# Kernel optimization log

Hardware: AMD Instinct MI355X
Metric: run time of the kernel (lower is better)

The kernel has to match this reference:

```python
import jax, jax.numpy as jnp
import numpy as np

VOCAB, DIM, HEADS, LAYERS = 32000, 1024, 16, 2
B, S = 2, 1024
HD = DIM // HEADS


def rmsnorm(x, g, eps=1e-6):
    return x * jax.lax.rsqrt(jnp.mean(x * x, axis=-1, keepdims=True) + eps) * g


def setup_inputs() -> dict:
    key = jax.random.key(0)
    ks = jax.random.split(key, 20)
    s = 0.02
    d = {
        "text_ids": jax.random.randint(ks[0], (B, S), 0, VOCAB),
        "embed": jax.random.normal(ks[1], (VOCAB, DIM), jnp.float32) * s,
        "g1": jnp.ones((LAYERS, DIM), jnp.float32),
        "wq": jax.random.normal(ks[2], (LAYERS, DIM, DIM), jnp.float32) * s,
        "bq": jnp.zeros((LAYERS, DIM), jnp.float32),
        "wk": jax.random.normal(ks[3], (LAYERS, DIM, DIM), jnp.float32) * s,
        "bk": jnp.zeros((LAYERS, DIM), jnp.float32),
        "wv": jax.random.normal(ks[4], (LAYERS, DIM, DIM), jnp.float32) * s,
        "bv": jnp.zeros((LAYERS, DIM), jnp.float32),
        "wo": jax.random.normal(ks[5], (LAYERS, DIM, DIM), jnp.float32) * s,
        "bo": jnp.zeros((LAYERS, DIM), jnp.float32),
        "g2": jnp.ones((LAYERS, DIM), jnp.float32),
        "w1": jax.random.normal(ks[6], (LAYERS, DIM, 4 * DIM), jnp.float32) * s,
        "b1": jnp.zeros((LAYERS, 4 * DIM), jnp.float32),
        "w2": jax.random.normal(ks[7], (LAYERS, 4 * DIM, DIM), jnp.float32) * s,
        "b2": jnp.zeros((LAYERS, DIM), jnp.float32),
        "gf": jnp.ones((DIM,), jnp.float32),
        "head_w": jax.random.normal(ks[8], (DIM, VOCAB), jnp.float32) * s,
        "head_b": jnp.zeros((VOCAB,), jnp.float32),
    }
    return d


def reference(text_ids, embed, g1, wq, bq, wk, bk, wv, bv, wo, bo,
              g2, w1, b1, w2, b2, gf, head_w, head_b):
    b, s = text_ids.shape
    x = embed[text_ids]                                   # [B,S,D]
    causal = jnp.tril(jnp.ones((s, s), dtype=bool))        # [S,S]
    scale = 1.0 / jnp.sqrt(jnp.asarray(HD, x.dtype))
    for l in range(LAYERS):
        # attention sublayer: x = x + attn(norm1(x))
        h = rmsnorm(x, g1[l])
        q = (h @ wq[l] + bq[l]).reshape(b, s, HEADS, HD)
        k = (h @ wk[l] + bk[l]).reshape(b, s, HEADS, HD)
        v = (h @ wv[l] + bv[l]).reshape(b, s, HEADS, HD)
        scores = jnp.einsum("bqhd,bkhd->bhqk", q, k) * scale
        scores = jnp.where(causal, scores, jnp.asarray(-1e30, scores.dtype))
        a = jax.nn.softmax(scores, axis=-1)
        o = jnp.einsum("bhqk,bkhd->bqhd", a, v).reshape(b, s, DIM)
        x = x + (o @ wo[l] + bo[l])
        # FFN sublayer: x = x + ffn(norm2(x)), SiLU MLP (MoE unused in source forward)
        h2 = rmsnorm(x, g2[l])
        x = x + (jax.nn.silu(h2 @ w1[l] + b1[l]) @ w2[l] + b2[l])
    x = rmsnorm(x, gf)
    return x.astype(jnp.float32) @ head_w + head_b         # [B,S,VOCAB]
```

## Files before the change

### kernel.cpp

```cpp
#include <hip/hip_runtime.h>

#define LAYERS 2
#define DIM 1024
#define HEADS 16
#define HD 64
#define BATCH 2
#define SEQ 1024
#define ROWS (BATCH * SEQ)
#define FFN (4 * DIM)
#define VOCAB 32000
#define QKVN (3 * DIM)

typedef unsigned short u16;
typedef short vshort8 __attribute__((ext_vector_type(8)));
typedef float f32x4 __attribute__((ext_vector_type(4)));

#define VMCNT(n) asm volatile("s_waitcnt vmcnt(" #n ")" ::: "memory")

__device__ __forceinline__ u16 f2bf(float f) {
  union { float f; unsigned u; } x{f};
  unsigned r = (x.u + 0x7fffu + ((x.u >> 16) & 1u)) >> 16;
  return (u16)r;
}

// ... 8 lines not shown
  int xcd = orig & 7;
  int base = (xcd < r) ? xcd * (q + 1) : r * (q + 1) + (xcd - r) * q;
  return base + (orig >> 3);
}

__device__ __forceinline__ void trans64(const float* __restrict__ src,
                                        u16* __restrict__ dst, int C, int R,
                                        int r0, int c0, int tid,
                                        u16 (*tl)[72]) {
  int lr = tid >> 4, lc4 = (tid & 15) * 4;
#pragma unroll
  for (int i = 0; i < 4; i++) {
    int row = lr + i * 16;
    float4 v = *(const float4*)&src[(size_t)(r0 + row) * C + c0 + lc4];
    ushort4 o{f2bf(v.x), f2bf(v.y), f2bf(v.z), f2bf(v.w)};
    *(ushort4*)&tl[row][lc4] = o;
  }
  __syncthreads();
#pragma unroll
  for (int i = 0; i < 2; i++) {
    int idx = tid + i * 256;
    int ci = idx >> 3, ri0 = (idx & 7) * 8;
    vshort8 o;
#pragma unroll
    for (int j = 0; j < 8; j++) o[j] = (short)tl[ri0 + j][ci];
    *(vshort8*)&dst[(size_t)(c0 + ci) * R + r0 + ri0] = o;
  }
}

__global__ __launch_bounds__(256) void transpose_all_kernel(
    const float* __restrict__ wq, const float* __restrict__ wk,
    const float* __restrict__ wv, const float* __restrict__ wo,
    const float* __restrict__ w1, const float* __restrict__ w2,
    const float* __restrict__ head_w, u16* __restrict__ wqkvT,
    u16* __restrict__ woT, u16* __restrict__ w1T, u16* __restrict__ w2T,
    u16* __restrict__ headT) {
  __shared__ u16 tl[64][72];
  int bid = blockIdx.x, tid = threadIdx.x;
  const float* src;
  u16* dst;
  int R, C, r0, c0;
  if (bid < 2048) {
    int job = bid >> 8, tile = bid & 255;
    int l = job >> 2, wsel = job & 3;
    src = (wsel == 0 ? wq : wsel == 1 ? wk : wsel == 2 ? wv : wo) +
          (size_t)l * DIM * DIM;
    dst = (wsel < 3)
              ? wqkvT + (size_t)l * QKVN * DIM + (size_t)wsel * DIM * DIM
              : woT + (size_t)l * DIM * DIM;
    R = DIM; C = DIM;
    c0 = (tile & 15) * 64; r0 = (tile >> 4) * 64;
  } else if (bid < 4096) {
    int idx = bid - 2048;
    int l = idx >> 10, t = idx & 1023;
    src = w1 + (size_t)l * DIM * FFN;
    dst = w1T + (size_t)l * DIM * FFN;
    R = DIM; C = FFN;
    c0 = (t & 63) * 64; r0 = (t >> 6) * 64;
  } else if (bid < 6144) {
    int idx = bid - 4096;
    int l = idx >> 10, t = idx & 1023;
    src = w2 + (size_t)l * FFN * DIM;
    dst = w2T + (size_t)l * FFN * DIM;
    R = FFN; C = DIM;
    c0 = (t & 15) * 64; r0 = (t >> 4) * 64;
  } else {
    int t = bid - 6144;
    src = head_w; dst = headT;
    R = DIM; C = VOCAB;
    c0 = (t % 500) * 64; r0 = (t / 500) * 64;
  }
  trans64(src, dst, C, R, r0, c0, tid, tl);
}

__global__ __launch_bounds__(256) void pack_qkv_bias(
    const float* __restrict__ bq, const float* __restrict__ bk,
    const float* __restrict__ bv, float* __restrict__ o) {
  int l = blockIdx.y;
  int t = blockIdx.x * 256 + threadIdx.x;
  float v;
  if (t < DIM) v = bq[l * DIM + t];
  else if (t < 2 * DIM) v = bk[l * DIM + t - DIM];
  else v = bv[l * DIM + t - 2 * DIM];
  o[(size_t)l * QKVN + t] = v;
}

__global__ __launch_bounds__(256) void embed_norm_kernel(
    const int* __restrict__ ids, const float* __restrict__ emb,
    const float* __restrict__ g, float* __restrict__ x, u16* __restrict__ h) {
  int row = blockIdx.x;
  int t = threadIdx.x;
  int id = ids[row];
  float4 v = ((const float4*)(emb + (size_t)id * DIM))[t];
  ((float4*)(x + (size_t)row * DIM))[t] = v;
  float ss = v.x * v.x + v.y * v.y + v.z * v.z + v.w * v.w;
  for (int off = 32; off > 0; off >>= 1) ss += __shfl_down(ss, off);
  __shared__ float part[4];
  if ((t & 63) == 0) part[t >> 6] = ss;
  __syncthreads();
  float tot = part[0] + part[1] + part[2] + part[3];
  float r = rsqrtf(tot / (float)DIM + 1e-6f);
  float4 gv = ((const float4*)g)[t];
  ushort4 o;
  o.x = f2bf(v.x * r * gv.x);
  o.y = f2bf(v.y * r * gv.y);
  o.z = f2bf(v.z * r * gv.z);
  o.w = f2bf(v.w * r * gv.w);
  *(ushort4*)(h + (size_t)row * DIM + t * 4) = o;
}

__global__ __launch_bounds__(256) void addnorm_kernel(
    float* __restrict__ x, const float* __restrict__ P0,
    const float* __restrict__ P1, const float* __restrict__ bias,
    const float* __restrict__ g, u16* __restrict__ h) {
  int row = blockIdx.x;
  int t = threadIdx.x;
  float4 v = ((const float4*)(x + (size_t)row * DIM))[t];
  float4 a = ((const float4*)(P0 + (size_t)row * DIM))[t];
  float4 b = ((const float4*)(P1 + (size_t)row * DIM))[t];
  float4 c = ((const float4*)bias)[t];
  v.x += a.x + b.x + c.x;
  v.y += a.y + b.y + c.y;
  v.z += a.z + b.z + c.z;
  v.w += a.w + b.w + c.w;
  ((float4*)(x + (size_t)row * DIM))[t] = v;
  float ss = v.x * v.x + v.y * v.y + v.z * v.z + v.w * v.w;
  for (int off = 32; off > 0; off >>= 1) ss += __shfl_down(ss, off);
  __shared__ float part[4];
  if ((t & 63) == 0) part[t >> 6] = ss;
  __syncthreads();
  float tot = part[0] + part[1] + part[2] + part[3];
  float r = rsqrtf(tot / (float)DIM + 1e-6f);
  float4 gv = ((const float4*)g)[t];
  ushort4 o;
  o.x = f2bf(v.x * r * gv.x);
  o.y = f2bf(v.y * r * gv.y);
  o.z = f2bf(v.z * r * gv.z);
  o.w = f2bf(v.w * r * gv.w);
  *(ushort4*)(h + (size_t)row * DIM + t * 4) = o;
}

template <int SILU, int VT>
__global__ __launch_bounds__(512, 2) void gemm256x128_kernel(
    const u16* __restrict__ A, const u16* __restrict__ Wt,
    const float* __restrict__ bias, u16* __restrict__ outb,
    u16* __restrict__ vt2, int M, int N, int K) {
  __shared__ u16 As[2][256 * 64];
  __shared__ u16 Bs[2][128 * 64];
  int nm = M >> 8, nn = N >> 7;
  int wg = xcd_swizzle(blockIdx.x, nm * nn);
  int mi = wg % nm, ni = wg / nm;
  int m0 = mi << 8, n0 = ni << 7;
  int tid = threadIdx.x, w = tid >> 6, lane = tid & 63;
  int wr = w >> 1, wc = w & 1;
  int r16 = lane & 15, g4 = lane >> 4;
  int srow8 = lane >> 3, sslot = lane & 7;
  int NT = K >> 6;

  f32x4 acc[4][4] = {};

  auto stageA = [&](int buf, int kt, int j) {
    int chunk = j * 8 + w;
    int row = chunk * 8 + srow8;
    int slot = sslot ^ (row & 7);
    gll16(A + (size_t)(m0 + row) * K + kt * 64 + slot * 8,
          &As[buf][chunk * 512 + lane * 8]);
  };
  auto stageB = [&](int buf, int kt, int j) {
    int chunk = j * 8 + w;
    int row = chunk * 8 + srow8;
    int slot = sslot ^ (row & 7);
    gll16(Wt + (size_t)(n0 + row) * K + kt * 64 + slot * 8,
          &Bs[buf][chunk * 512 + lane * 8]);
  };
  auto readA = [&](int buf, int mf, int kk) -> vshort8 {
    int row = wr * 64 + mf * 16 + r16;
    int slot = (kk * 4 + g4) ^ (row & 7);
    return *(const vshort8*)&As[buf][row * 64 + slot * 8];
  };
  auto readB = [&](int buf, int nf, int kk) -> vshort8 {
    int row = wc * 64 + nf * 16 + r16;
    int slot = (kk * 4 + g4) ^ (row & 7);
    return *(const vshort8*)&Bs[buf][row * 64 + slot * 8];
  };

  stageA(0, 0, 0); stageA(0, 0, 1); stageA(0, 0, 2); stageA(0, 0, 3);
  stageB(0, 0, 0); stageB(0, 0, 1);
  VMCNT(0);
  __builtin_amdgcn_s_barrier();

  vshort8 af[4][2], bf[2][2];

  for (int t = 0; t < NT; t++) {
    int cur = t & 1, nxt = cur ^ 1;
    bool hn = (t + 1 < NT);
#pragma unroll
    for (int m = 0; m < 4; m++)
#pragma unroll
      for (int kk = 0; kk < 2; kk++) af[m][kk] = readA(cur, m, kk);
#pragma unroll
    for (int n = 0; n < 2; n++)
#pragma unroll
      for (int kk = 0; kk < 2; kk++) bf[n][kk] = readB(cur, n, kk);
    if (hn) {
      stageA(nxt, t + 1, 0); stageA(nxt, t + 1, 1);
      stageA(nxt, t + 1, 2); stageA(nxt, t + 1, 3);
      stageB(nxt, t + 1, 0); stageB(nxt, t + 1, 1);
    }
    __builtin_amdgcn_s_barrier();
    __builtin_amdgcn_s_setprio(1);
#pragma unroll
    for (int m = 0; m < 4; m++)
#pragma unroll
      for (int n = 0; n < 2; n++)
#pragma unroll
        for (int kk = 0; kk < 2; kk++)
          acc[m][n] = __builtin_amdgcn_mfma_f32_16x16x32_bf16(
              af[m][kk], bf[n][kk], acc[m][n], 0, 0, 0);
    __builtin_amdgcn_s_setprio(0);
    __builtin_amdgcn_s_barrier();
#pragma unroll
    for (int n = 0; n < 2; n++)
#pragma unroll
      for (int kk = 0; kk < 2; kk++) bf[n][kk] = readB(cur, 2 + n, kk);
    __builtin_amdgcn_s_barrier();
    __builtin_amdgcn_s_setprio(1);
#pragma unroll
    for (int m = 0; m < 4; m++)
#pragma unroll
      for (int n = 0; n < 2; n++)
#pragma unroll
        for (int kk = 0; kk < 2; kk++)
          acc[m][n + 2] = __builtin_amdgcn_mfma_f32_16x16x32_bf16(
              af[m][kk], bf[n][kk], acc[m][n + 2], 0, 0, 0);
    __builtin_amdgcn_s_setprio(0);
    VMCNT(0);
    __builtin_amdgcn_s_barrier();
  }

#pragma unroll
  for (int m = 0; m < 4; m++) {
    int rowb = m0 + wr * 64 + m * 16 + g4 * 4;
#pragma unroll
    for (int n = 0; n < 4; n++) {
      int col = n0 + wc * 64 + n * 16 + r16;
      float b = bias[col];
      u16 ov[4];
#pragma unroll
      for (int j = 0; j < 4; j++) {
        float v = acc[m][n][j] + b;
        if (SILU) v = v / (1.f + __expf(-v));
        ov[j] = f2bf(v);
      }
      if (VT && col >= 2 * DIM) {
        int dv = col - 2 * DIM;
        int hh = dv >> 6, dd = dv & 63;
        int bb = rowb >> 10, s = rowb & 1023;
        ushort4 o4{ov[0], ov[1], ov[2], ov[3]};
        *(ushort4*)&vt2[((((size_t)(bb * 16 + hh) * (SEQ / 8) + (s >> 3)) * 64 +
                          dd) * 8) + (s & 7)] = o4;
      } else {
#pragma unroll
        for (int j = 0; j < 4; j++)
          outb[(size_t)(rowb + j) * N + col] = ov[j];
      }
    }
  }
}

template <int OUTBF, int SILU, int SPLITK, int MFAST, int VT>
__global__ __launch_bounds__(256, 2) void gemm128_kernel(
    const u16* __restrict__ A, const u16* __restrict__ Wt,
    const float* __restrict__ bias, void* __restrict__ outv,
    float* __restrict__ pout1, u16* __restrict__ vt2, int M, int N, int K) {
  __shared__ u16 As[2][128 * 64];
  __shared__ u16 Bs[2][128 * 64];
  int nm = M >> 7, nn = N >> 7, nwg = nm * nn;
  int wg = xcd_swizzle(blockIdx.x, SPLITK ? nwg * 2 : nwg);
  int ks = 0;
  if (SPLITK) { ks = wg >= nwg; wg -= ks * nwg; }
  int mi, ni;
  if (MFAST) { mi = wg % nm; ni = wg / nm; }
  else       { ni = wg % nn; mi = wg / nn; }
  int m0 = mi << 7, n0 = ni << 7;
  int kb = SPLITK ? ks * (K >> 1) : 0;
  int NTt = (SPLITK ? (K >> 1) : K) >> 6;
  int tid = threadIdx.x, wave = tid >> 6, lane = tid & 63;
  int wr = wave >> 1, wc = wave & 1;
  int r16 = lane & 15, g4 = lane >> 4;
  int lrow = lane >> 3, lslot = lane & 7;

  f32x4 acc[4][4] = {};

  auto stage = [&](int buf, int kt) {
#pragma unroll
    for (int i = 0; i < 4; i++) {
      int s = wave * 4 + i;
      int row = s * 8 + lrow;
      int slot = lslot ^ (row & 7);
      gll16(A + (size_t)(m0 + row) * K + kb + kt * 64 + slot * 8,
            &As[buf][s * 512 + lane * 8]);
    }
#pragma unroll
    for (int i = 0; i < 4; i++) {
      int s = wave * 4 + i;
      int row = s * 8 + lrow;
      int slot = lslot ^ (row & 7);
// ... 26 lines not shown
      }
#pragma unroll
      for (int m = 0; m < 4; m++)
#pragma unroll
        for (int n = 0; n < 4; n++)
          acc[m][n] = __builtin_amdgcn_mfma_f32_16x16x32_bf16(af[m], bf[n],
                                                              acc[m][n], 0, 0, 0);
    }
    VMCNT(0);
    __builtin_amdgcn_s_barrier();
  }

  if (SPLITK) {
    float* P = ks ? pout1 : (float*)outv;
#pragma unroll
    for (int m = 0; m < 4; m++) {
      int rowb = m0 + wr * 64 + m * 16 + g4 * 4;
#pragma unroll
      for (int n = 0; n < 4; n++) {
        int col = n0 + wc * 64 + n * 16 + r16;
#pragma unroll
        for (int j = 0; j < 4; j++)
          P[(size_t)(rowb + j) * N + col] = acc[m][n][j];
      }
    }
  } else {
#pragma unroll
    for (int m = 0; m < 4; m++) {
      int rowb = m0 + wr * 64 + m * 16 + g4 * 4;
#pragma unroll
      for (int n = 0; n < 4; n++) {
        int col = n0 + wc * 64 + n * 16 + r16;
        float b = bias[col];
        u16 ov[4];
#pragma unroll
        for (int j = 0; j < 4; j++) {
          float v = acc[m][n][j] + b;
          if (SILU) v = v / (1.f + __expf(-v));
          if (OUTBF) ov[j] = f2bf(v);
          else ((float*)outv)[(size_t)(rowb + j) * N + col] = v;
        }
        if (OUTBF) {
          if (VT && col >= 2 * DIM) {
            int dv = col - 2 * DIM;
            int hh = dv >> 6, dd = dv & 63;
            int bb = rowb >> 10, s = rowb & 1023;
            ushort4 o4{ov[0], ov[1], ov[2], ov[3]};
            *(ushort4*)&vt2[((((size_t)(bb * 16 + hh) * (SEQ / 8) + (s >> 3)) * 64 +
                              dd) * 8) + (s & 7)] = o4;
          } else {
#pragma unroll
            for (int j = 0; j < 4; j++)
              ((u16*)outv)[(size_t)(rowb + j) * N + col] = ov[j];
          }
        }
      }
    }
  }
}

__global__ __launch_bounds__(512, 2) void gemm256p_kernel(
    const u16* __restrict__ A, const u16* __restrict__ Wt,
    const float* __restrict__ bias, float* __restrict__ out,
    int M, int N, int K) {
  __shared__ u16 As[2][256 * 64];
  __shared__ u16 Bs[2][256 * 64];
  int nn = N >> 8;
  int wg = xcd_swizzle(blockIdx.x, nn * 2);
  int ni = wg >> 1, mhalf = wg & 1;
  int n0 = ni << 8;
  int tid = threadIdx.x, w = tid >> 6, lane = tid & 63;
  int wr = w >> 2, wc = w & 3;
  int r16 = lane & 15, g4 = lane >> 4;
  int srow8 = lane >> 3, sslot = lane & 7;
  const int NTK = 16;
  const int NGT = 64;

  f32x4 acc[8][4] = {};

  auto stageA = [&](int buf, int mb, int kt, int hb, int j) {
    int chunk = j * 8 + w;
    int row = hb * 128 + chunk * 8 + srow8;
    int slot = sslot ^ (row & 7);
    gll16(A + (size_t)(mb + row) * K + kt * 64 + slot * 8,
          &As[buf][hb * 8192 + chunk * 512 + lane * 8]);
  };
  auto stageB = [&](int buf, int kt, int hb, int j) {
    int chunk = j * 8 + w;
    int row = hb * 128 + chunk * 8 + srow8;
    int slot = sslot ^ (row & 7);
    gll16(Wt + (size_t)(n0 + row) * K + kt * 64 + slot * 8,
          &Bs[buf][hb * 8192 + chunk * 512 + lane * 8]);
  };
  auto readA = [&](int buf, int mf, int kk) -> vshort8 {
    int row = mf * 32 + wr * 16 + r16;
    int slot = (kk * 4 + g4) ^ (row & 7);
    return *(const vshort8*)&As[buf][row * 64 + slot * 8];
  };
  auto readB = [&](int buf, int nf, int kk) -> vshort8 {
    int row = nf * 64 + wc * 16 + r16;
    int slot = (kk * 4 + g4) ^ (row & 7);
    return *(const vshort8*)&Bs[buf][row * 64 + slot * 8];
  };

  int mb0 = (mhalf * 4) << 8;
  stageA(0, mb0, 0, 0, 0); stageA(0, mb0, 0, 0, 1);
  stageB(0, 0, 0, 0);      stageB(0, 0, 0, 1);
  stageB(0, 0, 1, 0);      stageB(0, 0, 1, 1);
  stageA(0, mb0, 0, 1, 0); stageA(0, mb0, 0, 1, 1);
  VMCNT(4);
  __builtin_amdgcn_s_barrier();

  vshort8 af[4][2], bf0[2][2], bf1[2][2];

  for (int ti = 0; ti < 4; ti++) {
    int m0 = (mhalf * 4 + ti) << 8;
    for (int tt = 0; tt < NTK; tt++) {
      int gt = ti * NTK + tt;
      int cur = gt & 1, nxt = cur ^ 1;
      int gt1 = gt + 1;
      bool hn = gt1 < NGT;
      int kt1 = gt1 & (NTK - 1);
      int mb1 = (mhalf * 4 + (gt1 >> 4)) << 8;
#pragma unroll
      for (int m = 0; m < 4; m++)
#pragma unroll
        for (int kk = 0; kk < 2; kk++) af[m][kk] = readA(cur, m, kk);
#pragma unroll
      for (int n = 0; n < 2; n++)
#pragma unroll
        for (int kk = 0; kk < 2; kk++) bf0[n][kk] = readB(cur, n, kk);
      if (hn) {
        stageA(nxt, mb1, kt1, 0, 0); stageA(nxt, mb1, kt1, 0, 1);
        stageB(nxt, kt1, 0, 0);      stageB(nxt, kt1, 0, 1);
      }
      __builtin_amdgcn_s_barrier();
      __builtin_amdgcn_s_setprio(1);
#pragma unroll
      for (int m = 0; m < 4; m++)
#pragma unroll
        for (int n = 0; n < 2; n++)
#pragma unroll
          for (int kk = 0; kk < 2; kk++)
            acc[m][n] = __builtin_amdgcn_mfma_f32_16x16x32_bf16(
                af[m][kk], bf0[n][kk], acc[m][n], 0, 0, 0);
      __builtin_amdgcn_s_setprio(0);
      VMCNT(4);
      __builtin_amdgcn_s_barrier();
#pragma unroll
      for (int n = 0; n < 2; n++)
#pragma unroll
        for (int kk = 0; kk < 2; kk++) bf1[n][kk] = readB(cur, 2 + n, kk);
      __builtin_amdgcn_s_barrier();
      __builtin_amdgcn_s_setprio(1);
#pragma unroll
      for (int m = 0; m < 4; m++)
#pragma unroll
        for (int n = 0; n < 2; n++)
#pragma unroll
          for (int kk = 0; kk < 2; kk++)
            acc[m][n + 2] = __builtin_amdgcn_mfma_f32_16x16x32_bf16(
                af[m][kk], bf1[n][kk], acc[m][n + 2], 0, 0, 0);
      __builtin_amdgcn_s_setprio(0);
      __builtin_amdgcn_s_barrier();
#pragma unroll
      for (int m = 0; m < 4; m++)
#pragma unroll
        for (int kk = 0; kk < 2; kk++) af[m][kk] = readA(cur, 4 + m, kk);
      if (hn) {
        stageB(nxt, kt1, 1, 0);      stageB(nxt, kt1, 1, 1);
        stageA(nxt, mb1, kt1, 1, 0); stageA(nxt, mb1, kt1, 1, 1);
      }
      __builtin_amdgcn_s_barrier();
      __builtin_amdgcn_s_setprio(1);
#pragma unroll
      for (int m = 0; m < 4; m++)
#pragma unroll
        for (int n = 0; n < 2; n++)
#pragma unroll
          for (int kk = 0; kk < 2; kk++)
            acc[m + 4][n + 2] = __builtin_amdgcn_mfma_f32_16x16x32_bf16(
                af[m][kk], bf1[n][kk], acc[m + 4][n + 2], 0, 0, 0);
#pragma unroll
      for (int m = 0; m < 4; m++)
#pragma unroll
        for (int n = 0; n < 2; n++)
#pragma unroll
          for (int kk = 0; kk < 2; kk++)
            acc[m + 4][n] = __builtin_amdgcn_mfma_f32_16x16x32_bf16(
                af[m][kk], bf0[n][kk], acc[m + 4][n], 0, 0, 0);
      __builtin_amdgcn_s_setprio(0);
      VMCNT(4);
      __builtin_amdgcn_s_barrier();
    }
#pragma unroll
    for (int mf = 0; mf < 8; mf++) {
      int rowb = m0 + mf * 32 + wr * 16 + g4 * 4;
#pragma unroll
      for (int nf = 0; nf < 4; nf++) {
        int col = n0 + nf * 64 + wc * 16 + r16;
        float b = bias[col];
#pragma unroll
        for (int j = 0; j < 4; j++)
          out[(size_t)(rowb + j) * N + col] = acc[mf][nf][j] + b;
      }
    }
#pragma unroll
    for (int mf = 0; mf < 8; mf++)
#pragma unroll
      for (int nf = 0; nf < 4; nf++) acc[mf][nf] = f32x4{0.f, 0.f, 0.f, 0.f};
  }
}

__global__ __launch_bounds__(256) void attn_kernel(const u16* __restrict__ qkv,
                                                   const u16* __restrict__ vt2,
                                                   u16* __restrict__ o) {
  __shared__ u16 Ks[2][32 * 64];
  __shared__ u16 pl[4][16 * 40];
  int qblk = blockIdx.x, bh = blockIdx.y;
  int b = bh >> 4, h = bh & 15;
  int tid = threadIdx.x, w = tid >> 6, lane = tid & 63;
  int r16 = lane & 15, g4 = lane >> 4;
  int q0 = qblk * 64 + w * 16;

  const u16* qrow = qkv + ((size_t)(b * SEQ) + q0 + r16) * QKVN + h * HD;
  vshort8 aq0 = *(const vshort8*)(qrow + g4 * 8);
  vshort8 aq1 = *(const vshort8*)(qrow + 32 + g4 * 8);

  float mrun[4], lrun[4];
  f32x4 accO[4];
#pragma unroll
  for (int j = 0; j < 4; j++) { mrun[j] = -1e30f; lrun[j] = 0.f; }
#pragma unroll
  for (int d = 0; d < 4; d++) accO[d] = f32x4{0.f, 0.f, 0.f, 0.f};

  int nkvT = qblk * 2 + 2;
  auto stageK = [&](int buf, int kt) {
    int row = tid >> 3;
    int slot = (tid & 7) ^ (row & 7);
    gll16(qkv + ((size_t)(b * SEQ) + kt * 32 + row) * QKVN + DIM + h * HD + slot * 8,
          &Ks[buf][w * 512 + lane * 8]);
  };
  stageK(0, 0);
// ... 79 lines not shown
  const float* g2 = (const float*)d_in[11];
  const float* w1 = (const float*)d_in[12];
  const float* b1 = (const float*)d_in[13];
  const float* w2 = (const float*)d_in[14];
  const float* b2 = (const float*)d_in[15];
  const float* gf = (const float*)d_in[16];
  const float* head_w = (const float*)d_in[17];
  const float* head_b = (const float*)d_in[18];
  float* out = (float*)d_out;

  char* ws = (char*)d_ws;
  size_t off = 0;
  auto alloc = [&](size_t bytes) -> char* {
    char* p = ws + off;
    off += (bytes + 255) & ~(size_t)255;
    return p;
  };
  u16* wqkvT = (u16*)alloc((size_t)LAYERS * QKVN * DIM * 2);
  u16* woT = (u16*)alloc((size_t)LAYERS * DIM * DIM * 2);
  u16* w1T = (u16*)alloc((size_t)LAYERS * DIM * FFN * 2);
  u16* w2T = (u16*)alloc((size_t)LAYERS * DIM * FFN * 2);
  u16* headT = (u16*)alloc((size_t)VOCAB * DIM * 2);
  float* bqkv = (float*)alloc((size_t)LAYERS * QKVN * 4);
  float* x = (float*)alloc((size_t)ROWS * DIM * 4);
  u16* h = (u16*)alloc((size_t)ROWS * DIM * 2);
  u16* qkvb = (u16*)alloc((size_t)ROWS * QKVN * 2);
  u16* vtb = (u16*)alloc((size_t)ROWS * DIM * 2);
  u16* ob = (u16*)alloc((size_t)ROWS * DIM * 2);
  u16* tb = (u16*)alloc((size_t)ROWS * FFN * 2);
  float* P0 = (float*)alloc((size_t)ROWS * DIM * 4);
  float* P1 = (float*)alloc((size_t)ROWS * DIM * 4);
  if (off > ws_size) return;

  transpose_all_kernel<<<14144, 256, 0, stream>>>(
      wq, wk, wv, wo, w1, w2, head_w, wqkvT, woT, w1T, w2T, headT);
  pack_qkv_bias<<<dim3(QKVN / 256, LAYERS), 256, 0, stream>>>(bq, bk, bv, bqkv);
  embed_norm_kernel<<<ROWS, 256, 0, stream>>>(ids, emb, g1, x, h);

  for (int l = 0; l < LAYERS; l++) {
    gemm256x128_kernel<0, 1>
        <<<(ROWS / 256) * (QKVN / 128), 512, 0, stream>>>(
            h, wqkvT + (size_t)l * QKVN * DIM, bqkv + (size_t)l * QKVN,
            qkvb, vtb, ROWS, QKVN, DIM);
    attn_kernel<<<dim3(SEQ / 64, BATCH * HEADS), 256, 0, stream>>>(qkvb, vtb, ob);
    gemm128_kernel<0, 0, 1, 0, 0>
        <<<2 * (ROWS / 128) * (DIM / 128), 256, 0, stream>>>(
            ob, woT + (size_t)l * DIM * DIM, nullptr, P0, P1, nullptr,
            ROWS, DIM, DIM);
    addnorm_kernel<<<ROWS, 256, 0, stream>>>(
        x, P0, P1, bo + (size_t)l * DIM, g2 + (size_t)l * DIM, h);
    gemm256x128_kernel<1, 0>
        <<<(ROWS / 256) * (FFN / 128), 512, 0, stream>>>(
            h, w1T + (size_t)l * DIM * FFN, b1 + (size_t)l * FFN, tb, nullptr,
            ROWS, FFN, DIM);
    gemm128_kernel<0, 0, 1, 0, 0>
        <<<2 * (ROWS / 128) * (DIM / 128), 256, 0, stream>>>(
            tb, w2T + (size_t)l * DIM * FFN, nullptr, P0, P1, nullptr,
            ROWS, DIM, FFN);
    addnorm_kernel<<<ROWS, 256, 0, stream>>>(
        x, P0, P1, b2 + (size_t)l * DIM,
        (l == LAYERS - 1) ? gf : (g1 + (size_t)(l + 1) * DIM), h);
  }
  gemm256p_kernel<<<(VOCAB / 256) * 2, 512, 0, stream>>>(
      h, headT, head_b, out, ROWS, VOCAB, DIM);
}
```

Baseline: 589.6 us.

## Triple-buffer 256x128 GEMM and reuse it persistently for the LM head

The 256x128 GEMM moves from double- to triple-buffered LDS, prefetching two K-tiles ahead with a partial vmcnt wait instead of a full drain every iteration. It also gains an NMT template parameter so one workgroup walks several M tiles for a fixed N column. The LM head now uses this kernel (NMT=8, 250 workgroups with 128-wide N tiles) in place of the dedicated 256x256 gemm256p kernel. Tripling LDS (144KB) may cut occupancy, and the head's smaller N tile lowers per-block reuse of the A operand.

```diff
diff --git a/kernel.cpp b/kernel.cpp
--- a/kernel.cpp
+++ b/kernel.cpp
@@ -172,38 +172,48 @@
   *(ushort4*)(h + (size_t)row * DIM + t * 4) = o;
 }
 
-template <int SILU, int VT>
-__global__ __launch_bounds__(512, 2) void gemm256x128_kernel(
+template <int NMT, int OUTF32, int SILU, int VT>
+__global__ __launch_bounds__(512, 2) void gemm256x128p_kernel(
     const u16* __restrict__ A, const u16* __restrict__ Wt,
-    const float* __restrict__ bias, u16* __restrict__ outb,
+    const float* __restrict__ bias, void* __restrict__ outv,
     u16* __restrict__ vt2, int M, int N, int K) {
-  __shared__ u16 As[2][256 * 64];
-  __shared__ u16 Bs[2][128 * 64];
+  __shared__ u16 As[3][256 * 64];
+  __shared__ u16 Bs[3][128 * 64];
   int nm = M >> 8, nn = N >> 7;
-  int wg = xcd_swizzle(blockIdx.x, nm * nn);
-  int mi = wg % nm, ni = wg / nm;
-  int m0 = mi << 8, n0 = ni << 7;
+  int nwg = (NMT == 1) ? nm * nn : nn;
+  int wg = xcd_swizzle(blockIdx.x, nwg);
+  int mi0, ni;
+  if (NMT == 1) { mi0 = wg % nm; ni = wg / nm; }
+  else          { mi0 = 0; ni = wg; }
+  int n0 = ni << 7;
   int tid = threadIdx.x, w = tid >> 6, lane = tid & 63;
   int wr = w >> 1, wc = w & 1;
   int r16 = lane & 15, g4 = lane >> 4;
   int srow8 = lane >> 3, sslot = lane & 7;
-  int NT = K >> 6;
+  const int NG = NMT * 16;
 
   f32x4 acc[4][4] = {};
 
-  auto stageA = [&](int buf, int kt, int j) {
-    int chunk = j * 8 + w;
-    int row = chunk * 8 + srow8;
-    int slot = sslot ^ (row & 7);
-    gll16(A + (size_t)(m0 + row) * K + kt * 64 + slot * 8,
-          &As[buf][chunk * 512 + lane * 8]);
-  };
-  auto stageB = [&](int buf, int kt, int j) {
-    int chunk = j * 8 + w;
-    int row = chunk * 8 + srow8;
-    int slot = sslot ^ (row & 7);
-    gll16(Wt + (size_t)(n0 + row) * K + kt * 64 + slot * 8,
-          &Bs[buf][chunk * 512 + lane * 8]);
+  auto stage = [&](int g) {
+    int buf = g % 3;
+    int kt = g & 15;
+    int mb = (mi0 + (g >> 4)) << 8;
+#pragma unroll
+    for (int j = 0; j < 4; j++) {
+      int chunk = j * 8 + w;
+      int row = chunk * 8 + srow8;
+      int slot = sslot ^ (row & 7);
+      gll16(A + (size_t)(mb + row) * K + kt * 64 + slot * 8,
+            &As[buf][chunk * 512 + lane * 8]);
+    }
+#pragma unroll
+    for (int j = 0; j < 2; j++) {
+      int chunk = j * 8 + w;
+      int row = chunk * 8 + srow8;
+      int slot = sslot ^ (row & 7);
+      gll16(Wt + (size_t)(n0 + row) * K + kt * 64 + slot * 8,
+            &Bs[buf][chunk * 512 + lane * 8]);
+    }
   };
   auto readA = [&](int buf, int mf, int kk) -> vshort8 {
     int row = wr * 64 + mf * 16 + r16;
@@ -216,85 +226,91 @@
     return *(const vshort8*)&Bs[buf][row * 64 + slot * 8];
   };
 
-  stageA(0, 0, 0); stageA(0, 0, 1); stageA(0, 0, 2); stageA(0, 0, 3);
-  stageB(0, 0, 0); stageB(0, 0, 1);
-  VMCNT(0);
+  stage(0);
+  stage(1);
+  VMCNT(6);
   __builtin_amdgcn_s_barrier();
 
-  vshort8 af[4][2], bf[2][2];
-
-  for (int t = 0; t < NT; t++) {
-    int cur = t & 1, nxt = cur ^ 1;
-    bool hn = (t + 1 < NT);
-#pragma unroll
-    for (int m = 0; m < 4; m++)
-#pragma unroll
-      for (int kk = 0; kk < 2; kk++) af[m][kk] = readA(cur, m, kk);
-#pragma unroll
-    for (int n = 0; n < 2; n++)
-#pragma unroll
-      for (int kk = 0; kk < 2; kk++) bf[n][kk] = readB(cur, n, kk);
-    if (hn) {
-      stageA(nxt, t + 1, 0); stageA(nxt, t + 1, 1);
-      stageA(nxt, t + 1, 2); stageA(nxt, t + 1, 3);
-      stageB(nxt, t + 1, 0); stageB(nxt, t + 1, 1);
-    }
-    __builtin_amdgcn_s_barrier();
-    __builtin_amdgcn_s_setprio(1);
-#pragma unroll
-    for (int m = 0; m < 4; m++)
+  vshort8 af[4][2], bf0[2][2], bf1[2][2];
+
+  for (int mt = 0; mt < NMT; mt++) {
+    for (int kt = 0; kt < 16; kt++) {
+      int g = mt * 16 + kt;
+      int buf = g % 3;
+#pragma unroll
+      for (int m = 0; m < 4; m++)
+#pragma unroll
+        for (int kk = 0; kk < 2; kk++) af[m][kk] = readA(buf, m, kk);
 #pragma unroll
       for (int n = 0; n < 2; n++)
 #pragma unroll
-        for (int kk = 0; kk < 2; kk++)
-          acc[m][n] = __builtin_amdgcn_mfma_f32_16x16x32_bf16(
-              af[m][kk], bf[n][kk], acc[m][n], 0, 0, 0);
-    __builtin_amdgcn_s_setprio(0);
-    __builtin_amdgcn_s_barrier();
-#pragma unroll
-    for (int n = 0; n < 2; n++)
-#pragma unroll
-      for (int kk = 0; kk < 2; kk++) bf[n][kk] = readB(cur, 2 + n, kk);
-    __builtin_amdgcn_s_barrier();
-    __builtin_amdgcn_s_setprio(1);
-#pragma unroll
-    for (int m = 0; m < 4; m++)
+        for (int kk = 0; kk < 2; kk++) bf0[n][kk] = readB(buf, n, kk);
+      bool staged = (g + 2 < NG);
+      if (staged) stage(g + 2);
+      __builtin_amdgcn_s_barrier();
+      __builtin_amdgcn_s_setprio(1);
+#pragma unroll
+      for (int m = 0; m < 4; m++)
+#pragma unroll
+        for (int n = 0; n < 2; n++)
+#pragma unroll
+          for (int kk = 0; kk < 2; kk++)
+            acc[m][n] = __builtin_amdgcn_mfma_f32_16x16x32_bf16(
+                af[m][kk], bf0[n][kk], acc[m][n], 0, 0, 0);
+      __builtin_amdgcn_s_setprio(0);
+      __builtin_amdgcn_s_barrier();
 #pragma unroll
       for (int n = 0; n < 2; n++)
 #pragma unroll
-        for (int kk = 0; kk < 2; kk++)
-          acc[m][n + 2] = __builtin_amdgcn_mfma_f32_16x16x32_bf16(
-              af[m][kk], bf[n][kk], acc[m][n + 2], 0, 0, 0);
-    __builtin_amdgcn_s_setprio(0);
-    VMCNT(0);
-    __builtin_amdgcn_s_barrier();
-  }
-
-#pragma unroll
-  for (int m = 0; m < 4; m++) {
-    int rowb = m0 + wr * 64 + m * 16 + g4 * 4;
-#pragma unroll
-    for (int n = 0; n < 4; n++) {
-      int col = n0 + wc * 64 + n * 16 + r16;
-      float b = bias[col];
-      u16 ov[4];
-#pragma unroll
-      for (int j = 0; j < 4; j++) {
-        float v = acc[m][n][j] + b;
-        if (SILU) v = v / (1.f + __expf(-v));
-        ov[j] = f2bf(v);
-      }
-      if (VT && col >= 2 * DIM) {
-        int dv = col - 2 * DIM;
-        int hh = dv >> 6, dd = dv & 63;
-        int bb = rowb >> 10, s = rowb & 1023;
-        ushort4 o4{ov[0], ov[1], ov[2], ov[3]};
-        *(ushort4*)&vt2[((((size_t)(bb * 16 + hh) * (SEQ / 8) + (s >> 3)) * 64 +
-                          dd) * 8) + (s & 7)] = o4;
-      } else {
-#pragma unroll
-        for (int j = 0; j < 4; j++)
-          outb[(size_t)(rowb + j) * N + col] = ov[j];
+        for (int kk = 0; kk < 2; kk++) bf1[n][kk] = readB(buf, 2 + n, kk);
+      __builtin_amdgcn_s_barrier();
+      __builtin_amdgcn_s_setprio(1);
+#pragma unroll
+      for (int m = 0; m < 4; m++)
+#pragma unroll
+        for (int n = 0; n < 2; n++)
+#pragma unroll
+          for (int kk = 0; kk < 2; kk++)
+            acc[m][n + 2] = __builtin_amdgcn_mfma_f32_16x16x32_bf16(
+                af[m][kk], bf1[n][kk], acc[m][n + 2], 0, 0, 0);
+      __builtin_amdgcn_s_setprio(0);
+      if (staged) { VMCNT(6); } else { VMCNT(0); }
+      __builtin_amdgcn_s_barrier();
+    }
+    int m0e = (mi0 + mt) << 8;
+#pragma unroll
+    for (int m = 0; m < 4; m++) {
+      int rowb = m0e + wr * 64 + m * 16 + g4 * 4;
+#pragma unroll
+      for (int n = 0; n < 4; n++) {
+        int col = n0 + wc * 64 + n * 16 + r16;
+        float b = bias[col];
+        if (OUTF32) {
+#pragma unroll
+          for (int j = 0; j < 4; j++)
+            ((float*)outv)[(size_t)(rowb + j) * N + col] = acc[m][n][j] + b;
+        } else {
+          u16 ov[4];
+#pragma unroll
+          for (int j = 0; j < 4; j++) {
+            float v = acc[m][n][j] + b;
+            if (SILU) v = v / (1.f + __expf(-v));
+            ov[j] = f2bf(v);
+          }
+          if (VT && col >= 2 * DIM) {
+            int dv = col - 2 * DIM;
+            int hh = dv >> 6, dd = dv & 63;
+            int bb = rowb >> 10, s = rowb & 1023;
+            ushort4 o4{ov[0], ov[1], ov[2], ov[3]};
+            *(ushort4*)&vt2[((((size_t)(bb * 16 + hh) * (SEQ / 8) + (s >> 3)) *
+                                  64 + dd) * 8) + (s & 7)] = o4;
+          } else {
+#pragma unroll
+            for (int j = 0; j < 4; j++)
+              ((u16*)outv)[(size_t)(rowb + j) * N + col] = ov[j];
+          }
+        }
+        if (NMT > 1) acc[m][n] = f32x4{0.f, 0.f, 0.f, 0.f};
       }
     }
   }
@@ -406,174 +422,12 @@
           else ((float*)outv)[(size_t)(rowb + j) * N + col] = v;
         }
         if (OUTBF) {
-          if (VT && col >= 2 * DIM) {
-            int dv = col - 2 * DIM;
-            int hh = dv >> 6, dd = dv & 63;
-            int bb = rowb >> 10, s = rowb & 1023;
-            ushort4 o4{ov[0], ov[1], ov[2], ov[3]};
-            *(ushort4*)&vt2[((((size_t)(bb * 16 + hh) * (SEQ / 8) + (s >> 3)) * 64 +
-                              dd) * 8) + (s & 7)] = o4;
-          } else {
-#pragma unroll
-            for (int j = 0; j < 4; j++)
-              ((u16*)outv)[(size_t)(rowb + j) * N + col] = ov[j];
-          }
+#pragma unroll
+          for (int j = 0; j < 4; j++)
+            ((u16*)outv)[(size_t)(rowb + j) * N + col] = ov[j];
         }
       }
     }
-  }
-}
-
-__global__ __launch_bounds__(512, 2) void gemm256p_kernel(
-    const u16* __restrict__ A, const u16* __restrict__ Wt,
-    const float* __restrict__ bias, float* __restrict__ out,
-    int M, int N, int K) {
-  __shared__ u16 As[2][256 * 64];
-  __shared__ u16 Bs[2][256 * 64];
-  int nn = N >> 8;
-  int wg = xcd_swizzle(blockIdx.x, nn * 2);
-  int ni = wg >> 1, mhalf = wg & 1;
-  int n0 = ni << 8;
-  int tid = threadIdx.x, w = tid >> 6, lane = tid & 63;
-  int wr = w >> 2, wc = w & 3;
-  int r16 = lane & 15, g4 = lane >> 4;
-  int srow8 = lane >> 3, sslot = lane & 7;
-  const int NTK = 16;
-  const int NGT = 64;
-
-  f32x4 acc[8][4] = {};
-
-  auto stageA = [&](int buf, int mb, int kt, int hb, int j) {
-    int chunk = j * 8 + w;
-    int row = hb * 128 + chunk * 8 + srow8;
-    int slot = sslot ^ (row & 7);
-    gll16(A + (size_t)(mb + row) * K + kt * 64 + slot * 8,
-          &As[buf][hb * 8192 + chunk * 512 + lane * 8]);
-  };
-  auto stageB = [&](int buf, int kt, int hb, int j) {
-    int chunk = j * 8 + w;
-    int row = hb * 128 + chunk * 8 + srow8;
-    int slot = sslot ^ (row & 7);
-    gll16(Wt + (size_t)(n0 + row) * K + kt * 64 + slot * 8,
-          &Bs[buf][hb * 8192 + chunk * 512 + lane * 8]);
-  };
-  auto readA = [&](int buf, int mf, int kk) -> vshort8 {
-    int row = mf * 32 + wr * 16 + r16;
-    int slot = (kk * 4 + g4) ^ (row & 7);
-    return *(const vshort8*)&As[buf][row * 64 + slot * 8];
-  };
-  auto readB = [&](int buf, int nf, int kk) -> vshort8 {
-    int row = nf * 64 + wc * 16 + r16;
-    int slot = (kk * 4 + g4) ^ (row & 7);
-    return *(const vshort8*)&Bs[buf][row * 64 + slot * 8];
-  };
-
-  int mb0 = (mhalf * 4) << 8;
-  stageA(0, mb0, 0, 0, 0); stageA(0, mb0, 0, 0, 1);
-  stageB(0, 0, 0, 0);      stageB(0, 0, 0, 1);
-  stageB(0, 0, 1, 0);      stageB(0, 0, 1, 1);
-  stageA(0, mb0, 0, 1, 0); stageA(0, mb0, 0, 1, 1);
-  VMCNT(4);
-  __builtin_amdgcn_s_barrier();
-
-  vshort8 af[4][2], bf0[2][2], bf1[2][2];
-
-  for (int ti = 0; ti < 4; ti++) {
-    int m0 = (mhalf * 4 + ti) << 8;
-    for (int tt = 0; tt < NTK; tt++) {
-      int gt = ti * NTK + tt;
-      int cur = gt & 1, nxt = cur ^ 1;
-      int gt1 = gt + 1;
-      bool hn = gt1 < NGT;
-      int kt1 = gt1 & (NTK - 1);
-      int mb1 = (mhalf * 4 + (gt1 >> 4)) << 8;
-#pragma unroll
-      for (int m = 0; m < 4; m++)
-#pragma unroll
-        for (int kk = 0; kk < 2; kk++) af[m][kk] = readA(cur, m, kk);
-#pragma unroll
-      for (int n = 0; n < 2; n++)
-#pragma unroll
-        for (int kk = 0; kk < 2; kk++) bf0[n][kk] = readB(cur, n, kk);
-      if (hn) {
-        stageA(nxt, mb1, kt1, 0, 0); stageA(nxt, mb1, kt1, 0, 1);
-        stageB(nxt, kt1, 0, 0);      stageB(nxt, kt1, 0, 1);
-      }
-      __builtin_amdgcn_s_barrier();
-      __builtin_amdgcn_s_setprio(1);
-#pragma unroll
-      for (int m = 0; m < 4; m++)
-#pragma unroll
-        for (int n = 0; n < 2; n++)
-#pragma unroll
-          for (int kk = 0; kk < 2; kk++)
-            acc[m][n] = __builtin_amdgcn_mfma_f32_16x16x32_bf16(
-                af[m][kk], bf0[n][kk], acc[m][n], 0, 0, 0);
-      __builtin_amdgcn_s_setprio(0);
-      VMCNT(4);
-      __builtin_amdgcn_s_barrier();
-#pragma unroll
-      for (int n = 0; n < 2; n++)
-#pragma unroll
-        for (int kk = 0; kk < 2; kk++) bf1[n][kk] = readB(cur, 2 + n, kk);
-      __builtin_amdgcn_s_barrier();
-      __builtin_amdgcn_s_setprio(1);
-#pragma unroll
-      for (int m = 0; m < 4; m++)
-#pragma unroll
-        for (int n = 0; n < 2; n++)
-#pragma unroll
-          for (int kk = 0; kk < 2; kk++)
-            acc[m][n + 2] = __builtin_amdgcn_mfma_f32_16x16x32_bf16(
-                af[m][kk], bf1[n][kk], acc[m][n + 2], 0, 0, 0);
-      __builtin_amdgcn_s_setprio(0);
-      __builtin_amdgcn_s_barrier();
-#pragma unroll
-      for (int m = 0; m < 4; m++)
-#pragma unroll
-        for (int kk = 0; kk < 2; kk++) af[m][kk] = readA(cur, 4 + m, kk);
-      if (hn) {
-        stageB(nxt, kt1, 1, 0);      stageB(nxt, kt1, 1, 1);
-        stageA(nxt, mb1, kt1, 1, 0); stageA(nxt, mb1, kt1, 1, 1);
-      }
-      __builtin_amdgcn_s_barrier();
-      __builtin_amdgcn_s_setprio(1);
-#pragma unroll
-      for (int m = 0; m < 4; m++)
-#pragma unroll
-        for (int n = 0; n < 2; n++)
-#pragma unroll
-          for (int kk = 0; kk < 2; kk++)
-            acc[m + 4][n + 2] = __builtin_amdgcn_mfma_f32_16x16x32_bf16(
-                af[m][kk], bf1[n][kk], acc[m + 4][n + 2], 0, 0, 0);
-#pragma unroll
-      for (int m = 0; m < 4; m++)
-#pragma unroll
-        for (int n = 0; n < 2; n++)
-#pragma unroll
-          for (int kk = 0; kk < 2; kk++)
-            acc[m + 4][n] = __builtin_amdgcn_mfma_f32_16x16x32_bf16(
-                af[m][kk], bf0[n][kk], acc[m + 4][n], 0, 0, 0);
-      __builtin_amdgcn_s_setprio(0);
-      VMCNT(4);
-      __builtin_amdgcn_s_barrier();
-    }
-#pragma unroll
-    for (int mf = 0; mf < 8; mf++) {
-      int rowb = m0 + mf * 32 + wr * 16 + g4 * 4;
-#pragma unroll
-      for (int nf = 0; nf < 4; nf++) {
-        int col = n0 + nf * 64 + wc * 16 + r16;
-        float b = bias[col];
-#pragma unroll
-        for (int j = 0; j < 4; j++)
-          out[(size_t)(rowb + j) * N + col] = acc[mf][nf][j] + b;
-      }
-    }
-#pragma unroll
-    for (int mf = 0; mf < 8; mf++)
-#pragma unroll
-      for (int nf = 0; nf < 4; nf++) acc[mf][nf] = f32x4{0.f, 0.f, 0.f, 0.f};
   }
 }
 
@@ -725,7 +579,7 @@
   embed_norm_kernel<<<ROWS, 256, 0, stream>>>(ids, emb, g1, x, h);
 
   for (int l = 0; l < LAYERS; l++) {
-    gemm256x128_kernel<0, 1>
+    gemm256x128p_kernel<1, 0, 0, 1>
         <<<(ROWS / 256) * (QKVN / 128), 512, 0, stream>>>(
             h, wqkvT + (size_t)l * QKVN * DIM, bqkv + (size_t)l * QKVN,
             qkvb, vtb, ROWS, QKVN, DIM);
@@ -736,7 +590,7 @@
             ROWS, DIM, DIM);
     addnorm_kernel<<<ROWS, 256, 0, stream>>>(
         x, P0, P1, bo + (size_t)l * DIM, g2 + (size_t)l * DIM, h);
-    gemm256x128_kernel<1, 0>
+    gemm256x128p_kernel<1, 0, 1, 0>
         <<<(ROWS / 256) * (FFN / 128), 512, 0, stream>>>(
             h, w1T + (size_t)l * DIM * FFN, b1 + (size_t)l * FFN, tb, nullptr,
             ROWS, FFN, DIM);
@@ -748,6 +602,6 @@
         x, P0, P1, b2 + (size_t)l * DIM,
         (l == LAYERS - 1) ? gf : (g1 + (size_t)(l + 1) * DIM), h);
   }
-  gemm256p_kernel<<<(VOCAB / 256) * 2, 512, 0, stream>>>(
-      h, headT, head_b, out, ROWS, VOCAB, DIM);
-}
+  gemm256x128p_kernel<8, 1, 0, 0><<<VOCAB / 128, 512, 0, stream>>>(
+      h, headT, head_b, out, nullptr, ROWS, VOCAB, DIM);
+}
```

Result: slower. 649.3 us (+10.1%).

## Triple-buffer the 256x128 GEMM pipeline and fold bias packing into transpose

Applied to the files above, without the earlier changes.

The 256x128 GEMM used for the QKV and FFN-up projections now keeps three LDS stages and prefetches two K-tiles ahead. It waits with a partial vmcnt instead of draining all loads every iteration, so global-to-LDS latency is hidden further behind the MFMA work. The QKV bias packing kernel is merged into the weight transpose launch as extra blocks, removing one kernel launch. The LM-head GEMM's workgroup-to-tile mapping changes so the two M halves are split by block range instead of interleaved, which alters cache locality across XCDs. The larger LDS footprint (144KB per block) limits residency to one block per CU, and an unused multi-M-tile template option is added.

```diff
diff --git a/kernel.cpp b/kernel.cpp
--- a/kernel.cpp
+++ b/kernel.cpp
@@ -64,11 +64,23 @@
     const float* __restrict__ wq, const float* __restrict__ wk,
     const float* __restrict__ wv, const float* __restrict__ wo,
     const float* __restrict__ w1, const float* __restrict__ w2,
-    const float* __restrict__ head_w, u16* __restrict__ wqkvT,
-    u16* __restrict__ woT, u16* __restrict__ w1T, u16* __restrict__ w2T,
-    u16* __restrict__ headT) {
+    const float* __restrict__ head_w, const float* __restrict__ bq,
+    const float* __restrict__ bk, const float* __restrict__ bv,
+    u16* __restrict__ wqkvT, u16* __restrict__ woT, u16* __restrict__ w1T,
+    u16* __restrict__ w2T, u16* __restrict__ headT,
+    float* __restrict__ bqkv) {
   __shared__ u16 tl[64][72];
   int bid = blockIdx.x, tid = threadIdx.x;
+  if (bid >= 14144) {
+    int t = (bid - 14144) * 256 + tid;
+    int l = t / QKVN, c = t % QKVN;
+    float v;
+    if (c < DIM) v = bq[l * DIM + c];
+    else if (c < 2 * DIM) v = bk[l * DIM + c - DIM];
+    else v = bv[l * DIM + c - 2 * DIM];
+    bqkv[(size_t)l * QKVN + c] = v;
+    return;
+  }
   const float* src;
   u16* dst;
   int R, C, r0, c0;
@@ -105,18 +117,6 @@
   trans64(src, dst, C, R, r0, c0, tid, tl);
 }
 
-__global__ __launch_bounds__(256) void pack_qkv_bias(
-    const float* __restrict__ bq, const float* __restrict__ bk,
-    const float* __restrict__ bv, float* __restrict__ o) {
-  int l = blockIdx.y;
-  int t = blockIdx.x * 256 + threadIdx.x;
-  float v;
-  if (t < DIM) v = bq[l * DIM + t];
-  else if (t < 2 * DIM) v = bk[l * DIM + t - DIM];
-  else v = bv[l * DIM + t - 2 * DIM];
-  o[(size_t)l * QKVN + t] = v;
-}
-
 __global__ __launch_bounds__(256) void embed_norm_kernel(
     const int* __restrict__ ids, const float* __restrict__ emb,
     const float* __restrict__ g, float* __restrict__ x, u16* __restrict__ h) {
@@ -172,38 +172,48 @@
   *(ushort4*)(h + (size_t)row * DIM + t * 4) = o;
 }
 
-template <int SILU, int VT>
-__global__ __launch_bounds__(512, 2) void gemm256x128_kernel(
+template <int NMT, int OUTF32, int SILU, int VT>
+__global__ __launch_bounds__(512, 2) void gemm256x128p_kernel(
     const u16* __restrict__ A, const u16* __restrict__ Wt,
-    const float* __restrict__ bias, u16* __restrict__ outb,
+    const float* __restrict__ bias, void* __restrict__ outv,
     u16* __restrict__ vt2, int M, int N, int K) {
-  __shared__ u16 As[2][256 * 64];
-  __shared__ u16 Bs[2][128 * 64];
+  __shared__ u16 As[3][256 * 64];
+  __shared__ u16 Bs[3][128 * 64];
   int nm = M >> 8, nn = N >> 7;
-  int wg = xcd_swizzle(blockIdx.x, nm * nn);
-  int mi = wg % nm, ni = wg / nm;
-  int m0 = mi << 8, n0 = ni << 7;
+  int nwg = (NMT == 1) ? nm * nn : nn;
+  int wg = xcd_swizzle(blockIdx.x, nwg);
+  int mi0, ni;
+  if (NMT == 1) { mi0 = wg % nm; ni = wg / nm; }
+  else          { mi0 = 0; ni = wg; }
+  int n0 = ni << 7;
   int tid = threadIdx.x, w = tid >> 6, lane = tid & 63;
   int wr = w >> 1, wc = w & 1;
   int r16 = lane & 15, g4 = lane >> 4;
   int srow8 = lane >> 3, sslot = lane & 7;
-  int NT = K >> 6;
+  const int NG = NMT * 16;
 
   f32x4 acc[4][4] = {};
 
-  auto stageA = [&](int buf, int kt, int j) {
-    int chunk = j * 8 + w;
-    int row = chunk * 8 + srow8;
-    int slot = sslot ^ (row & 7);
-    gll16(A + (size_t)(m0 + row) * K + kt * 64 + slot * 8,
-          &As[buf][chunk * 512 + lane * 8]);
-  };
-  auto stageB = [&](int buf, int kt, int j) {
-    int chunk = j * 8 + w;
-    int row = chunk * 8 + srow8;
-    int slot = sslot ^ (row & 7);
-    gll16(Wt + (size_t)(n0 + row) * K + kt * 64 + slot * 8,
-          &Bs[buf][chunk * 512 + lane * 8]);
+  auto stage = [&](int g) {
+    int buf = g % 3;
+    int kt = g & 15;
+    int mb = (mi0 + (g >> 4)) << 8;
+#pragma unroll
+    for (int j = 0; j < 4; j++) {
+      int chunk = j * 8 + w;
+      int row = chunk * 8 + srow8;
+      int slot = sslot ^ (row & 7);
+      gll16(A + (size_t)(mb + row) * K + kt * 64 + slot * 8,
+            &As[buf][chunk * 512 + lane * 8]);
+    }
+#pragma unroll
+    for (int j = 0; j < 2; j++) {
+      int chunk = j * 8 + w;
+      int row = chunk * 8 + srow8;
+      int slot = sslot ^ (row & 7);
+      gll16(Wt + (size_t)(n0 + row) * K + kt * 64 + slot * 8,
+            &Bs[buf][chunk * 512 + lane * 8]);
+    }
   };
   auto readA = [&](int buf, int mf, int kk) -> vshort8 {
     int row = wr * 64 + mf * 16 + r16;
@@ -216,95 +226,101 @@
     return *(const vshort8*)&Bs[buf][row * 64 + slot * 8];
   };
 
-  stageA(0, 0, 0); stageA(0, 0, 1); stageA(0, 0, 2); stageA(0, 0, 3);
-  stageB(0, 0, 0); stageB(0, 0, 1);
-  VMCNT(0);
+  stage(0);
+  stage(1);
+  VMCNT(6);
   __builtin_amdgcn_s_barrier();
 
-  vshort8 af[4][2], bf[2][2];
-
-  for (int t = 0; t < NT; t++) {
-    int cur = t & 1, nxt = cur ^ 1;
-    bool hn = (t + 1 < NT);
-#pragma unroll
-    for (int m = 0; m < 4; m++)
-#pragma unroll
-      for (int kk = 0; kk < 2; kk++) af[m][kk] = readA(cur, m, kk);
-#pragma unroll
-    for (int n = 0; n < 2; n++)
-#pragma unroll
-      for (int kk = 0; kk < 2; kk++) bf[n][kk] = readB(cur, n, kk);
-    if (hn) {
-      stageA(nxt, t + 1, 0); stageA(nxt, t + 1, 1);
-      stageA(nxt, t + 1, 2); stageA(nxt, t + 1, 3);
-      stageB(nxt, t + 1, 0); stageB(nxt, t + 1, 1);
-    }
-    __builtin_amdgcn_s_barrier();
-    __builtin_amdgcn_s_setprio(1);
-#pragma unroll
-    for (int m = 0; m < 4; m++)
+  vshort8 af[4][2], bf0[2][2], bf1[2][2];
+
+  for (int mt = 0; mt < NMT; mt++) {
+    for (int kt = 0; kt < 16; kt++) {
+      int g = mt * 16 + kt;
+      int buf = g % 3;
+#pragma unroll
+      for (int m = 0; m < 4; m++)
+#pragma unroll
+        for (int kk = 0; kk < 2; kk++) af[m][kk] = readA(buf, m, kk);
 #pragma unroll
       for (int n = 0; n < 2; n++)
 #pragma unroll
-        for (int kk = 0; kk < 2; kk++)
-          acc[m][n] = __builtin_amdgcn_mfma_f32_16x16x32_bf16(
-              af[m][kk], bf[n][kk], acc[m][n], 0, 0, 0);
-    __builtin_amdgcn_s_setprio(0);
-    __builtin_amdgcn_s_barrier();
-#pragma unroll
-    for (int n = 0; n < 2; n++)
-#pragma unroll
-      for (int kk = 0; kk < 2; kk++) bf[n][kk] = readB(cur, 2 + n, kk);
-    __builtin_amdgcn_s_barrier();
-    __builtin_amdgcn_s_setprio(1);
-#pragma unroll
-    for (int m = 0; m < 4; m++)
+        for (int kk = 0; kk < 2; kk++) bf0[n][kk] = readB(buf, n, kk);
+      bool staged = (g + 2 < NG);
+      if (staged) stage(g + 2);
+      __builtin_amdgcn_s_barrier();
+      __builtin_amdgcn_s_setprio(1);
+#pragma unroll
+      for (int m = 0; m < 4; m++)
+#pragma unroll
+        for (int n = 0; n < 2; n++)
+#pragma unroll
+          for (int kk = 0; kk < 2; kk++)
+            acc[m][n] = __builtin_amdgcn_mfma_f32_16x16x32_bf16(
+                af[m][kk], bf0[n][kk], acc[m][n], 0, 0, 0);
+      __builtin_amdgcn_s_setprio(0);
+      __builtin_amdgcn_s_barrier();
 #pragma unroll
       for (int n = 0; n < 2; n++)
 #pragma unroll
-        for (int kk = 0; kk < 2; kk++)
-          acc[m][n + 2] = __builtin_amdgcn_mfma_f32_16x16x32_bf16(
-              af[m][kk], bf[n][kk], acc[m][n + 2], 0, 0, 0);
-    __builtin_amdgcn_s_setprio(0);
-    VMCNT(0);
-    __builtin_amdgcn_s_barrier();
-  }
-
-#pragma unroll
-  for (int m = 0; m < 4; m++) {
-    int rowb = m0 + wr * 64 + m * 16 + g4 * 4;
-#pragma unroll
-    for (int n = 0; n < 4; n++) {
-      int col = n0 + wc * 64 + n * 16 + r16;
-      float b = bias[col];
-      u16 ov[4];
-#pragma unroll
-      for (int j = 0; j < 4; j++) {
-        float v = acc[m][n][j] + b;
-        if (SILU) v = v / (1.f + __expf(-v));
-        ov[j] = f2bf(v);
-      }
-      if (VT && col >= 2 * DIM) {
-        int dv = col - 2 * DIM;
-        int hh = dv >> 6, dd = dv & 63;
-        int bb = rowb >> 10, s = rowb & 1023;
-        ushort4 o4{ov[0], ov[1], ov[2], ov[3]};
-        *(ushort4*)&vt2[((((size_t)(bb * 16 + hh) * (SEQ / 8) + (s >> 3)) * 64 +
-                          dd) * 8) + (s & 7)] = o4;
-      } else {
-#pragma unroll
-        for (int j = 0; j < 4; j++)
-          outb[(size_t)(rowb + j) * N + col] = ov[j];
-      }
-    }
-  }
-}
-
-template <int OUTBF, int SILU, int SPLITK, int MFAST, int VT>
+        for (int kk = 0; kk < 2; kk++) bf1[n][kk] = readB(buf, 2 + n, kk);
+      __builtin_amdgcn_s_barrier();
+      __builtin_amdgcn_s_setprio(1);
+#pragma unroll
+      for (int m = 0; m < 4; m++)
+#pragma unroll
+        for (int n = 0; n < 2; n++)
+#pragma unroll
+          for (int kk = 0; kk < 2; kk++)
+            acc[m][n + 2] = __builtin_amdgcn_mfma_f32_16x16x32_bf16(
+                af[m][kk], bf1[n][kk], acc[m][n + 2], 0, 0, 0);
+      __builtin_amdgcn_s_setprio(0);
+      if (staged) { VMCNT(6); } else { VMCNT(0); }
+      __builtin_amdgcn_s_barrier();
+    }
+    int m0e = (mi0 + mt) << 8;
+#pragma unroll
+    for (int m = 0; m < 4; m++) {
+      int rowb = m0e + wr * 64 + m * 16 + g4 * 4;
+#pragma unroll
+      for (int n = 0; n < 4; n++) {
+        int col = n0 + wc * 64 + n * 16 + r16;
+        float b = bias[col];
+        if (OUTF32) {
+#pragma unroll
+          for (int j = 0; j < 4; j++)
+            ((float*)outv)[(size_t)(rowb + j) * N + col] = acc[m][n][j] + b;
+        } else {
+          u16 ov[4];
+#pragma unroll
+          for (int j = 0; j < 4; j++) {
+            float v = acc[m][n][j] + b;
+            if (SILU) v = v / (1.f + __expf(-v));
+            ov[j] = f2bf(v);
+          }
+          if (VT && col >= 2 * DIM) {
+            int dv = col - 2 * DIM;
+            int hh = dv >> 6, dd = dv & 63;
+            int bb = rowb >> 10, s = rowb & 1023;
+            ushort4 o4{ov[0], ov[1], ov[2], ov[3]};
+            *(ushort4*)&vt2[((((size_t)(bb * 16 + hh) * (SEQ / 8) + (s >> 3)) *
+                                  64 + dd) * 8) + (s & 7)] = o4;
+          } else {
+#pragma unroll
+            for (int j = 0; j < 4; j++)
+              ((u16*)outv)[(size_t)(rowb + j) * N + col] = ov[j];
+          }
+        }
+        if (NMT > 1) acc[m][n] = f32x4{0.f, 0.f, 0.f, 0.f};
+      }
+    }
+  }
+}
+
+template <int OUTBF, int SILU, int SPLITK, int MFAST>
 __global__ __launch_bounds__(256, 2) void gemm128_kernel(
     const u16* __restrict__ A, const u16* __restrict__ Wt,
     const float* __restrict__ bias, void* __restrict__ outv,
-    float* __restrict__ pout1, u16* __restrict__ vt2, int M, int N, int K) {
+    float* __restrict__ pout1, int M, int N, int K) {
   __shared__ u16 As[2][128 * 64];
   __shared__ u16 Bs[2][128 * 64];
   int nm = M >> 7, nn = N >> 7, nwg = nm * nn;
@@ -397,27 +413,14 @@
       for (int n = 0; n < 4; n++) {
         int col = n0 + wc * 64 + n * 16 + r16;
         float b = bias[col];
-        u16 ov[4];
 #pragma unroll
         for (int j = 0; j < 4; j++) {
           float v = acc[m][n][j] + b;
           if (SILU) v = v / (1.f + __expf(-v));
-          if (OUTBF) ov[j] = f2bf(v);
-          else ((float*)outv)[(size_t)(rowb + j) * N + col] = v;
-        }
-        if (OUTBF) {
-          if (VT && col >= 2 * DIM) {
-            int dv = col - 2 * DIM;
-            int hh = dv >> 6, dd = dv & 63;
-            int bb = rowb >> 10, s = rowb & 1023;
-            ushort4 o4{ov[0], ov[1], ov[2], ov[3]};
-            *(ushort4*)&vt2[((((size_t)(bb * 16 + hh) * (SEQ / 8) + (s >> 3)) * 64 +
-                              dd) * 8) + (s & 7)] = o4;
-          } else {
-#pragma unroll
-            for (int j = 0; j < 4; j++)
-              ((u16*)outv)[(size_t)(rowb + j) * N + col] = ov[j];
-          }
+          if (OUTBF)
+            ((u16*)outv)[(size_t)(rowb + j) * N + col] = f2bf(v);
+          else
+            ((float*)outv)[(size_t)(rowb + j) * N + col] = v;
         }
       }
     }
@@ -432,7 +435,8 @@
   __shared__ u16 Bs[2][256 * 64];
   int nn = N >> 8;
   int wg = xcd_swizzle(blockIdx.x, nn * 2);
-  int ni = wg >> 1, mhalf = wg & 1;
+  int mhalf = wg >= nn;
+  int ni = mhalf ? wg - nn : wg;
   int n0 = ni << 8;
   int tid = threadIdx.x, w = tid >> 6, lane = tid & 63;
   int wr = w >> 2, wc = w & 3;
@@ -719,31 +723,29 @@
   float* P1 = (float*)alloc((size_t)ROWS * DIM * 4);
   if (off > ws_size) return;
 
-  transpose_all_kernel<<<14144, 256, 0, stream>>>(
-      wq, wk, wv, wo, w1, w2, head_w, wqkvT, woT, w1T, w2T, headT);
-  pack_qkv_bias<<<dim3(QKVN / 256, LAYERS), 256, 0, stream>>>(bq, bk, bv, bqkv);
+  transpose_all_kernel<<<14144 + 24, 256, 0, stream>>>(
+      wq, wk, wv, wo, w1, w2, head_w, bq, bk, bv, wqkvT, woT, w1T, w2T, headT,
+      bqkv);
   embed_norm_kernel<<<ROWS, 256, 0, stream>>>(ids, emb, g1, x, h);
 
   for (int l = 0; l < LAYERS; l++) {
-    gemm256x128_kernel<0, 1>
+    gemm256x128p_kernel<1, 0, 0, 1>
         <<<(ROWS / 256) * (QKVN / 128), 512, 0, stream>>>(
             h, wqkvT + (size_t)l * QKVN * DIM, bqkv + (size_t)l * QKVN,
             qkvb, vtb, ROWS, QKVN, DIM);
     attn_kernel<<<dim3(SEQ / 64, BATCH * HEADS), 256, 0, stream>>>(qkvb, vtb, ob);
-    gemm128_kernel<0, 0, 1, 0, 0>
+    gemm128_kernel<0, 0, 1, 0>
         <<<2 * (ROWS / 128) * (DIM / 128), 256, 0, stream>>>(
-            ob, woT + (size_t)l * DIM * DIM, nullptr, P0, P1, nullptr,
-            ROWS, DIM, DIM);
+            ob, woT + (size_t)l * DIM * DIM, nullptr, P0, P1, ROWS, DIM, DIM);
     addnorm_kernel<<<ROWS, 256, 0, stream>>>(
         x, P0, P1, bo + (size_t)l * DIM, g2 + (size_t)l * DIM, h);
-    gemm256x128_kernel<1, 0>
+    gemm256x128p_kernel<1, 0, 1, 0>
         <<<(ROWS / 256) * (FFN / 128), 512, 0, stream>>>(
             h, w1T + (size_t)l * DIM * FFN, b1 + (size_t)l * FFN, tb, nullptr,
             ROWS, FFN, DIM);
-    gemm128_kernel<0, 0, 1, 0, 0>
+    gemm128_kernel<0, 0, 1, 0>
         <<<2 * (ROWS / 128) * (DIM / 128), 256, 0, stream>>>(
-            tb, w2T + (size_t)l * DIM * FFN, nullptr, P0, P1, nullptr,
-            ROWS, DIM, FFN);
+            tb, w2T + (size_t)l * DIM * FFN, nullptr, P0, P1, ROWS, DIM, FFN);
     addnorm_kernel<<<ROWS, 256, 0, stream>>>(
         x, P0, P1, b2 + (size_t)l * DIM,
         (l == LAYERS - 1) ? gf : (g1 + (size_t)(l + 1) * DIM), h);
```

Result: no change. 591.4 us (+0.3%).
